# Kernel optimization log

Measured on AMD Instinct MI355X. Metric: run time of the kernel, lower is better.

The kernel has to match this reference:

```python
import jax, jax.numpy as jnp
import numpy as np

B, D_IN, UNITS = 8192, 4096, 4096

def setup_inputs() -> dict:
    key = jax.random.key(0)
    k1, k2 = jax.random.split(key)
    x = jax.random.normal(k1, (B, D_IN), dtype=jnp.float32)
    kernel = jax.random.normal(k2, (D_IN, UNITS), dtype=jnp.float32) * 0.02  # glorot-ish scale
    bias = jnp.zeros((UNITS,), dtype=jnp.float32)
    return {"x": x, "kernel": kernel, "bias": bias}

def reference(x, kernel, bias):
    # BinaryDense: binarize weights via sign, then dense matmul + bias
    kernel_bin = jnp.sign(kernel)                     # [D_IN, UNITS], values in {-1,0,+1}
    out = jnp.matmul(x, kernel_bin) + bias            # [B, UNITS]
    return out
```

## Files before the change

### kernel.cpp

```cpp
#include <hip/hip_runtime.h>
#include <stdint.h>


typedef int int4v __attribute__((ext_vector_type(4)));
typedef int int16v __attribute__((ext_vector_type(16)));

constexpr int M = 8192, N = 4096, K = 4096;
constexpr int BM = 256, BN = 256, BK = 128;
constexpr int NT = K / BK;

__device__ __forceinline__ void gload_lds16(const void* g, void* l) {
  __builtin_amdgcn_global_load_lds(
      (const __attribute__((address_space(1))) unsigned int*)g,
      (__attribute__((address_space(3))) unsigned int*)l, 16, 0, 0);
}

#define FENCE asm volatile("" ::: "memory")

__global__ __launch_bounds__(256) void prep_kernel(const float* __restrict__ x,
                                                   signed char* __restrict__ xq,
                                                   float* __restrict__ rscale,
                                                   const float* __restrict__ w,
                                                   signed char* __restrict__ wq) {
  const int t = threadIdx.x;
  if (blockIdx.x < M) {
    const int row = blockIdx.x;
    const float* xr = x + (size_t)row * K;
    float4 v[4];
    float mx = 0.f;
#pragma unroll
    for (int i = 0; i < 4; ++i) {
      v[i] = *(const float4*)(xr + t * 16 + i * 4);
      mx = fmaxf(mx, fmaxf(fmaxf(fabsf(v[i].x), fabsf(v[i].y)),
                           fmaxf(fabsf(v[i].z), fabsf(v[i].w))));
    }
#pragma unroll
    for (int off = 32; off >= 1; off >>= 1)
      mx = fmaxf(mx, __shfl_xor(mx, off, 64));
    __shared__ float smax[4];
    if ((t & 63) == 0) smax[t >> 6] = mx;
    __syncthreads();
    const float rm = fmaxf(fmaxf(smax[0], smax[1]), fmaxf(smax[2], smax[3]));
    const float s = (rm > 0.f) ? 127.f / rm : 0.f;
    if (t == 0) rscale[row] = (rm > 0.f) ? rm / 127.f : 0.f;
    uint32_t o[4];
#pragma unroll
    for (int i = 0; i < 4; ++i) {
      float f[4] = {v[i].x, v[i].y, v[i].z, v[i].w};
      uint32_t p = 0;
#pragma unroll
      for (int j = 0; j < 4; ++j) {
        int q = (int)rintf(f[j] * s);
        p |= ((uint32_t)(uint8_t)(signed char)q) << (8 * j);
      }
      o[i] = p;
    }
    *(int4v*)(xq + (size_t)row * K + t * 16) =
        (int4v){(int)o[0], (int)o[1], (int)o[2], (int)o[3]};
  } else {
    __shared__ __align__(16) signed char tile[64 * 68];
    const int idx = blockIdx.x - M;
    const int n0 = (idx & 63) * 64, k0 = (idx >> 6) * 64;
#pragma unroll
    for (int i = 0; i < 4; ++i) {
      int kl = (t >> 4) + i * 16;
      int nl = (t & 15) * 4;
      float4 v = *(const float4*)(w + (size_t)(k0 + kl) * N + n0 + nl);
      uint32_t p = 0;
      p |= ((uint32_t)(uint8_t)(signed char)((v.x > 0.f) - (v.x < 0.f)));
      p |= ((uint32_t)(uint8_t)(signed char)((v.y > 0.f) - (v.y < 0.f))) << 8;
      p |= ((uint32_t)(uint8_t)(signed char)((v.z > 0.f) - (v.z < 0.f))) << 16;
      p |= ((uint32_t)(uint8_t)(signed char)((v.w > 0.f) - (v.w < 0.f))) << 24;
      *(uint32_t*)(tile + kl * 68 + nl) = p;
    }
    __syncthreads();
    const int nl = t >> 2;
    const int kc = (t & 3) * 16;
    uint32_t o[4] = {0, 0, 0, 0};
#pragma unroll
    for (int j = 0; j < 16; ++j)
      o[j >> 2] |= ((uint32_t)(uint8_t)tile[(kc + j) * 68 + nl]) << (8 * (j & 3));
    *(int4v*)(wq + (size_t)(n0 + nl) * K + k0 + kc) =
        (int4v){(int)o[0], (int)o[1], (int)o[2], (int)o[3]};
  }
}


#define RD_SET(AN, BN_, P, KK)                                                    \
  {                                                                               \
    _Pragma("unroll") for (int mi_ = 0; mi_ < 4; ++mi_) {                         \
      const int r_ = wm * 128 + mi_ * 32 + l31;                                   \
      AN[mi_] = *(const int4v*)(smem + (P)*65536 + r_ * 128 +                     \
                                ((((KK)*2 + hi) ^ (r_ & 7)) * 16));               \
    }                                                                             \
    _Pragma("unroll") for (int ni_ = 0; ni_ < 2; ++ni_) {                         \
      const int r_ = wn * 64 + ni_ * 32 + l31;                                    \
      BN_[ni_] = *(const int4v*)(smem + (P)*65536 + 32768 + r_ * 128 +            \
                                 ((((KK)*2 + hi) ^ (r_ & 7)) * 16));              \
    }                                                                             \
  }

#define MM(AN, BN_)                                                               \
  {                                                                               \
    __builtin_amdgcn_s_setprio(1);                                                \
    _Pragma("unroll") for (int mi_ = 0; mi_ < 4; ++mi_) {                         \
      _Pragma("unroll") for (int ni_ = 0; ni_ < 2; ++ni_) {                       \
        acc[mi_][ni_] = __builtin_amdgcn_mfma_i32_32x32x32_i8(                    \
            AN[mi_], BN_[ni_], acc[mi_][ni_], 0, 0, 0);                           \
      }                                                                           \
    }                                                                             \
    __builtin_amdgcn_s_setprio(0);                                                \
  }

#define TILE(P, NP, TS, MORE)                                                     \
  {                                                                               \
    RD_SET(aY, bY, P, 1);                                                         \
    if (MORE) stage(NP, TS);                                                      \
    MM(aX, bX);                                                           \
    RD_SET(aX, bX, P, 2);                                                         \
    MM(aY, bY);                                                           \
    RD_SET(aY, bY, P, 3);                                                         \
    MM(aX, bX);                                                           \
    asm volatile("s_waitcnt vmcnt(0)" ::: "memory");                              \
    __builtin_amdgcn_s_barrier();                                                 \
    FENCE;                                                                        \
    if (MORE) RD_SET(aX, bX, NP, 0);                                              \
    MM(aY, bY);                                                           \
    FENCE;                                                                        \
    __builtin_amdgcn_s_barrier();                                                 \
    FENCE;                                                                        \
  }

__global__ __launch_bounds__(512, 2) void gemm_bin_kernel(
    const signed char* __restrict__ Xq,
    const signed char* __restrict__ Wq,
    const float* __restrict__ rscale,
    const float* __restrict__ bias,
    float* __restrict__ out) {
  __shared__ __align__(16) signed char smem[131072];

  const int tid = threadIdx.x;
  const int w = tid >> 6;
  const int lane = tid & 63;
  const int wm = w >> 2;
  const int wn = w & 3;
  const int hi = lane >> 5;
  const int l31 = lane & 31;
  const size_t m0 = (size_t)blockIdx.y * BM;
  const size_t n0 = (size_t)blockIdx.x * BN;

  int16v acc[4][2];
#pragma unroll
  for (int i = 0; i < 4; ++i)
#pragma unroll
    for (int j = 0; j < 2; ++j)
#pragma unroll
      for (int r = 0; r < 16; ++r) acc[i][j][r] = 0;
  int4v aX[4], bX[2], aY[4], bY[2];

  auto stage = [&](int pb, int t) {
    signed char* lb = smem + pb * 65536;
#pragma unroll
    for (int it = 0; it < 4; ++it) {
      int pos = it * 512 + tid;
      int row = pos >> 3, s = pos & 7;
      int qg = s ^ (row & 7);
      gload_lds16(Xq + (m0 + row) * (size_t)K + (size_t)t * BK + qg * 16,
                  lb + row * 128 + s * 16);
    }
#pragma unroll
    for (int it = 0; it < 4; ++it) {
      int pos = it * 512 + tid;
      int row = pos >> 3, s = pos & 7;
      int qg = s ^ (row & 7);
      gload_lds16(Wq + (n0 + row) * (size_t)K + (size_t)t * BK + qg * 16,
                  lb + 32768 + row * 128 + s * 16);
    }
  };

  stage(0, 0);
  asm volatile("s_waitcnt vmcnt(0)" ::: "memory");
  __builtin_amdgcn_s_barrier();
  FENCE;
  RD_SET(aX, bX, 0, 0);

#pragma unroll 1
  for (int tt = 0; tt < NT; tt += 2) {
    TILE(0, 1, tt + 1, true)
    TILE(1, 0, tt + 2, (tt + 2 < NT))
  }

#pragma unroll
  for (int mi = 0; mi < 4; ++mi) {
    const size_t rbase = m0 + wm * 128 + mi * 32;
    float sc[4][4];
#pragma unroll
    for (int q = 0; q < 4; ++q)
      *(float4*)sc[q] = *(const float4*)(rscale + rbase + hi * 4 + q * 8);
#pragma unroll
    for (int ni = 0; ni < 2; ++ni) {
      const size_t col = n0 + wn * 64 + ni * 32 + l31;
      const float bv = bias[col];
#pragma unroll
      for (int r = 0; r < 16; ++r) {
        const int row = (r & 3) + 8 * (r >> 2) + 4 * hi;
        out[(rbase + row) * N + col] = (float)acc[mi][ni][r] * sc[r >> 2][r & 3] + bv;
      }
    }
  }
}

extern "C" void kernel_launch(void* const* d_in, const int* in_sizes, int n_in,
                              void* d_out, int out_size, void* d_ws, size_t ws_size,
                              hipStream_t stream) {
  const float* x = (const float*)d_in[0];
  const float* kern = (const float*)d_in[1];
  const float* bias = (const float*)d_in[2];
  float* out = (float*)d_out;

  signed char* Xq = (signed char*)d_ws;
  signed char* Wq = Xq + (size_t)M * K;
  float* rscale = (float*)(Wq + (size_t)N * K);

  prep_kernel<<<M + (N / 64) * (K / 64), 256, 0, stream>>>(x, Xq, rscale, kern, Wq);
  gemm_bin_kernel<<<dim3(N / BN, M / BM), 512, 0, stream>>>(Xq, Wq, rscale, bias, out);
}
```

Before: 391.0 us.

## Switch int8 GEMM to a four-stage LDS ring with BK 64 and prefetch two ahead

Halves the K tile to 64 and splits the same 128 KB of LDS into four 32 KB stages used as a ring buffer. Global-to-LDS loads are issued two tiles ahead. A partial vmcnt wait lets the newest prefetch stay in flight, and each tile needs one barrier instead of two. The XOR swizzle is reworked for the 64-byte rows. The aim is to hide global load latency and cut barrier stalls between the MFMA bursts, at the cost of more loop iterations, less MFMA work per barrier and a new LDS bank-conflict pattern.

```diff
diff --git a/kernel.cpp b/kernel.cpp
--- a/kernel.cpp
+++ b/kernel.cpp
@@ -6,7 +6,7 @@
 typedef int int16v __attribute__((ext_vector_type(16)));
 
 constexpr int M = 8192, N = 4096, K = 4096;
-constexpr int BM = 256, BN = 256, BK = 128;
+constexpr int BM = 256, BN = 256, BK = 64;
 constexpr int NT = K / BK;
 
 __device__ __forceinline__ void gload_lds16(const void* g, void* l) {
@@ -86,49 +86,49 @@
 }
 
 
-#define RD_SET(AN, BN_, P, KK)                                                    \
-  {                                                                               \
-    _Pragma("unroll") for (int mi_ = 0; mi_ < 4; ++mi_) {                         \
-      const int r_ = wm * 128 + mi_ * 32 + l31;                                   \
-      AN[mi_] = *(const int4v*)(smem + (P)*65536 + r_ * 128 +                     \
-                                ((((KK)*2 + hi) ^ (r_ & 7)) * 16));               \
-    }                                                                             \
-    _Pragma("unroll") for (int ni_ = 0; ni_ < 2; ++ni_) {                         \
-      const int r_ = wn * 64 + ni_ * 32 + l31;                                    \
-      BN_[ni_] = *(const int4v*)(smem + (P)*65536 + 32768 + r_ * 128 +            \
-                                 ((((KK)*2 + hi) ^ (r_ & 7)) * 16));              \
-    }                                                                             \
-  }
-
-#define MM(AN, BN_)                                                               \
-  {                                                                               \
-    __builtin_amdgcn_s_setprio(1);                                                \
-    _Pragma("unroll") for (int mi_ = 0; mi_ < 4; ++mi_) {                         \
-      _Pragma("unroll") for (int ni_ = 0; ni_ < 2; ++ni_) {                       \
-        acc[mi_][ni_] = __builtin_amdgcn_mfma_i32_32x32x32_i8(                    \
-            AN[mi_], BN_[ni_], acc[mi_][ni_], 0, 0, 0);                           \
-      }                                                                           \
-    }                                                                             \
-    __builtin_amdgcn_s_setprio(0);                                                \
-  }
-
-#define TILE(P, NP, TS, MORE)                                                     \
-  {                                                                               \
-    RD_SET(aY, bY, P, 1);                                                         \
-    if (MORE) stage(NP, TS);                                                      \
-    MM(aX, bX);                                                           \
-    RD_SET(aX, bX, P, 2);                                                         \
-    MM(aY, bY);                                                           \
-    RD_SET(aY, bY, P, 3);                                                         \
-    MM(aX, bX);                                                           \
-    asm volatile("s_waitcnt vmcnt(0)" ::: "memory");                              \
-    __builtin_amdgcn_s_barrier();                                                 \
-    FENCE;                                                                        \
-    if (MORE) RD_SET(aX, bX, NP, 0);                                              \
-    MM(aY, bY);                                                           \
-    FENCE;                                                                        \
-    __builtin_amdgcn_s_barrier();                                                 \
-    FENCE;                                                                        \
+#define RD_SET(AN, BN_, P, KK)                                                 \
+  {                                                                            \
+    _Pragma("unroll") for (int mi_ = 0; mi_ < 4; ++mi_) {                      \
+      const int r_ = wm * 128 + mi_ * 32 + l31;                                \
+      const int sl_ = ((KK)*2 + hi) ^ ((r_ >> 1) & 3);                         \
+      AN[mi_] = *(const int4v*)(smem + (P)*32768 + r_ * 64 + sl_ * 16);        \
+    }                                                                          \
+    _Pragma("unroll") for (int ni_ = 0; ni_ < 2; ++ni_) {                      \
+      const int r_ = wn * 64 + ni_ * 32 + l31;                                 \
+      const int sl_ = ((KK)*2 + hi) ^ ((r_ >> 1) & 3);                         \
+      BN_[ni_] = *(const int4v*)(smem + (P)*32768 + 16384 + r_ * 64 +          \
+                                 sl_ * 16);                                    \
+    }                                                                          \
+  }
+
+#define MM(AN, BN_)                                                            \
+  {                                                                            \
+    __builtin_amdgcn_s_setprio(1);                                             \
+    _Pragma("unroll") for (int mi_ = 0; mi_ < 4; ++mi_) {                      \
+      _Pragma("unroll") for (int ni_ = 0; ni_ < 2; ++ni_) {                    \
+        acc[mi_][ni_] = __builtin_amdgcn_mfma_i32_32x32x32_i8(                 \
+            AN[mi_], BN_[ni_], acc[mi_][ni_], 0, 0, 0);                        \
+      }                                                                        \
+    }                                                                          \
+    __builtin_amdgcn_s_setprio(0);                                             \
+  }
+
+#define TILE(P, Q, S, T)                                                       \
+  {                                                                            \
+    RD_SET(aY, bY, P, 1);                                                      \
+    const bool more2_ = (T) + 2 < NT;                                          \
+    if (more2_) stage(S, (T) + 2);                                             \
+    MM(aX, bX);                                                                \
+    if (more2_) {                                                              \
+      asm volatile("s_waitcnt vmcnt(4)" ::: "memory");                         \
+    } else {                                                                   \
+      asm volatile("s_waitcnt vmcnt(0)" ::: "memory");                         \
+    }                                                                          \
+    __builtin_amdgcn_s_barrier();                                              \
+    FENCE;                                                                     \
+    if ((T) + 1 < NT) RD_SET(aX, bX, Q, 0);                                    \
+    MM(aY, bY);                                                                \
+    FENCE;                                                                     \
   }
 
 __global__ __launch_bounds__(512, 2) void gemm_bin_kernel(
@@ -159,35 +159,38 @@
   int4v aX[4], bX[2], aY[4], bY[2];
 
   auto stage = [&](int pb, int t) {
-    signed char* lb = smem + pb * 65536;
-#pragma unroll
-    for (int it = 0; it < 4; ++it) {
+    signed char* lb = smem + pb * 32768;
+#pragma unroll
+    for (int it = 0; it < 2; ++it) {
       int pos = it * 512 + tid;
-      int row = pos >> 3, s = pos & 7;
-      int qg = s ^ (row & 7);
+      int row = pos >> 2, s = pos & 3;
+      int qg = s ^ ((row >> 1) & 3);
       gload_lds16(Xq + (m0 + row) * (size_t)K + (size_t)t * BK + qg * 16,
-                  lb + row * 128 + s * 16);
-    }
-#pragma unroll
-    for (int it = 0; it < 4; ++it) {
+                  lb + pos * 16);
+    }
+#pragma unroll
+    for (int it = 0; it < 2; ++it) {
       int pos = it * 512 + tid;
-      int row = pos >> 3, s = pos & 7;
-      int qg = s ^ (row & 7);
+      int row = pos >> 2, s = pos & 3;
+      int qg = s ^ ((row >> 1) & 3);
       gload_lds16(Wq + (n0 + row) * (size_t)K + (size_t)t * BK + qg * 16,
-                  lb + 32768 + row * 128 + s * 16);
+                  lb + 16384 + pos * 16);
     }
   };
 
   stage(0, 0);
-  asm volatile("s_waitcnt vmcnt(0)" ::: "memory");
+  stage(1, 1);
+  asm volatile("s_waitcnt vmcnt(4)" ::: "memory");
   __builtin_amdgcn_s_barrier();
   FENCE;
   RD_SET(aX, bX, 0, 0);
 
 #pragma unroll 1
-  for (int tt = 0; tt < NT; tt += 2) {
-    TILE(0, 1, tt + 1, true)
-    TILE(1, 0, tt + 2, (tt + 2 < NT))
+  for (int t = 0; t < NT; t += 4) {
+    TILE(0, 1, 2, t)
+    TILE(1, 2, 3, t + 1)
+    TILE(2, 3, 0, t + 2)
+    TILE(3, 0, 1, t + 3)
   }
 
 #pragma unroll
```

Result: no change. 392.5 us (+0.4%).
